# Kernel tuning notes

Measured on AMD Instinct MI355X. Metric: run time of the kernel, lower is better.

Reference implementation:

```python
import jax, jax.numpy as jnp
import numpy as np

NSAMPLE = 32
EPS = 1e-5

def _conv1x1(x, W, b):
    # x: (B, Cin, M, K), W: (Cout, Cin) -> (B, Cout, M, K)
    return jnp.einsum('oc,bcmk->bomk', W, x) + b[None, :, None, None]

def _bn(x, g, b):
    # BatchNorm2d in train mode: per-channel batch stats over (B, M, K)
    mu = x.mean(axis=(0, 2, 3), keepdims=True)
    var = ((x - mu) ** 2).mean(axis=(0, 2, 3), keepdims=True)
    return (x - mu) * jax.lax.rsqrt(var + EPS) * g[None, :, None, None] + b[None, :, None, None]

def setup_inputs() -> dict:
    key = jax.random.key(0)
    ks = jax.random.split(key, 8)
    B, P, C = 4, 8192, 64
    hidden, out_ch = 128, 128
    in_tot = C + 3
    w = lambda k, shape: jax.random.normal(k, shape, jnp.float32) * 0.05
    return {
        'xyz': jax.random.normal(ks[0], (B, P, 3), jnp.float32),
        'feats': jax.random.normal(ks[1], (B, C, P), jnp.float32),
        'W1': w(ks[2], (hidden, in_tot)), 'b1': jnp.zeros((hidden,), jnp.float32),
        'g1': jnp.ones((hidden,), jnp.float32), 'be1': jnp.zeros((hidden,), jnp.float32),
        'W2': w(ks[3], (out_ch, hidden)), 'b2': jnp.zeros((out_ch,), jnp.float32),
        'g2': jnp.ones((out_ch,), jnp.float32), 'be2': jnp.zeros((out_ch,), jnp.float32),
        'Wq1': w(ks[4], (out_ch // 2, out_ch)), 'bq1': jnp.zeros((out_ch // 2,), jnp.float32),
        'Wq2': w(ks[5], (1, out_ch // 2)), 'bq2': jnp.zeros((1,), jnp.float32),
    }

def reference(xyz, feats, W1, b1, g1, be1, W2, b2, g2, be2, Wq1, bq1, Wq2, bq2):
    B, P, _ = xyz.shape
    M = max(1, P // 4)
    K = min(NSAMPLE, P)
    # deterministic equispaced centers (torch.linspace(...).long() truncates = floor)
    idx_c = jnp.floor(jnp.linspace(0.0, P - 1.0, M)).astype(jnp.int32)
    centers = jnp.take(xyz, idx_c, axis=1)                      # (B, M, 3)
    # squared pairwise distances (same argsort order as cdist)
    d2 = ((centers ** 2).sum(-1)[:, :, None]
          + (xyz ** 2).sum(-1)[:, None, :]
          - 2.0 * jnp.einsum('bmd,bnd->bmn', centers, xyz))     # (B, M, P)
    _, idx = jax.lax.top_k(-d2, K)                              # (B, M, K) nearest
    gather = jax.vmap(lambda pts, i: pts[i])                    # (B,P,C),(B,M,K)->(B,M,K,C)
    neigh_xyz = gather(xyz, idx)                                # (B, M, K, 3)
    local_xyz = jnp.transpose(neigh_xyz - centers[:, :, None, :], (0, 3, 1, 2))  # (B,3,M,K)
    neigh_f = jnp.transpose(gather(jnp.swapaxes(feats, 1, 2), idx), (0, 3, 1, 2))  # (B,C,M,K)
    cat = jnp.concatenate([local_xyz, neigh_f], axis=1)         # (B, C+3, M, K)
    h = jax.nn.relu(_bn(_conv1x1(cat, W1, b1), g1, be1))
    feat_local = jax.nn.relu(_bn(_conv1x1(h, W2, b2), g2, be2))  # (B, out_ch, M, K)
    w = _conv1x1(jax.nn.relu(_conv1x1(feat_local, Wq1, bq1)), Wq2, bq2)  # (B,1,M,K)
    w = jax.nn.softmax(w, axis=-1)
    feat_agg = (feat_local * w).sum(-1)                         # (B, out_ch, M)
    return centers, feat_agg
```

## Files before the change

### kernel.cpp

```cpp
#include <hip/hip_runtime.h>


typedef __attribute__((ext_vector_type(8))) short s16x8;
typedef __attribute__((ext_vector_type(4))) float f32x4;

__device__ __forceinline__ unsigned short f2bf(float f) {
  unsigned int u = __float_as_uint(f);
  unsigned int r = u + 0x7fffu + ((u >> 16) & 1u);
  return (unsigned short)(r >> 16);
}
__device__ __forceinline__ float bf2f(unsigned short s) {
  return __uint_as_float(((unsigned int)s) << 16);
}

__global__ __launch_bounds__(256) void prep2_kernel(const float* __restrict__ W1,
                                                    const float* __restrict__ W2,
                                                    const float* __restrict__ Wq1,
                                                    const float* __restrict__ xyz,
                                                    const float* __restrict__ feats,
                                                    unsigned short* __restrict__ W1p,
                                                    unsigned short* __restrict__ W2p,
                                                    unsigned short* __restrict__ Wq1p,
                                                    float4* __restrict__ xyzq,
                                                    unsigned short* __restrict__ featsT) {
  __shared__ float tile[64][65];
  const int t = threadIdx.x;
  if (blockIdx.x >= 282) {
    const int bx = blockIdx.x - 282;
    const int b = bx >> 7;
    const int p0 = (bx & 127) * 64;
    {
      const int pp = t & 63, c4 = t >> 6;
#pragma unroll
      for (int j = 0; j < 16; ++j) {
        int c = j * 4 + c4;
        tile[c][pp] = feats[((size_t)(b * 64 + c)) * 8192 + p0 + pp];
      }
    }
    __syncthreads();
    {
      const int cc = t & 63, p4 = t >> 6;
#pragma unroll
      for (int j = 0; j < 16; ++j) {
        int pr = j * 4 + p4;
        featsT[((size_t)(b * 8192 + p0 + pr)) * 64 + cc] = f2bf(tile[cc][pr]);
      }
    }
    return;
  }
  int i = blockIdx.x * 256 + t;
  if (i < 13312) {
    int o = i / 104, k = i % 104;
    float v = 0.f;
    if (k < 64) v = W1[o * 67 + 3 + k];
    else if (k < 67) v = W1[o * 67 + (k - 64)];
    W1p[i] = f2bf(v);
    return;
  }
  i -= 13312;
  if (i < 17408) {
    int o = i / 136, k = i % 136;
    W2p[i] = (k < 128) ? f2bf(W2[o * 128 + k]) : (unsigned short)0;
    return;
  }
  i -= 17408;
  if (i < 8704) {
    int o = i / 136, k = i % 136;
    Wq1p[i] = (k < 128) ? f2bf(Wq1[o * 128 + k]) : (unsigned short)0;
    return;
  }
  i -= 8704;
  if (i < 32768) {
    const float* q = xyz + (size_t)i * 3;
    float x = q[0], y = q[1], z = q[2];
    float4 v; v.x = x; v.y = y; v.z = z; v.w = (x * x + y * y) + z * z;
    xyzq[i] = v;
  }
}

#define CANDMAX 512
__global__ __launch_bounds__(512, 2) void sel3_kernel(const float4* __restrict__ xyzq,
    float* __restrict__ centers_out, int* __restrict__ idx_out) {
  const int t = threadIdx.x, lane = t & 63, wid = t >> 6;
  const int b = blockIdx.y;
  const int m0 = blockIdx.x * 16;
  __shared__ unsigned int hist[2][4096];
  __shared__ unsigned long long cand[2][CANDMAX];
  __shared__ float4 cc4[16];
  __shared__ int selb[2][32];
  __shared__ int ctrl[2][2];
  __shared__ int cutb[2];
  __shared__ int wsum[2][4];

  const float4* xb = xyzq + (size_t)b * 8192;
  float4 pt[16];
#pragma unroll
  for (int i = 0; i < 16; ++i) pt[i] = xb[i * 512 + t];

  if (t < 16) {
    int mIdx = m0 + t;
    int pc = (mIdx * 8191) / 2047;
    float4 c = xb[pc];
    cc4[t] = c;
    float* co = centers_out + ((size_t)(b * 2048 + mIdx)) * 3;
    co[0] = c.x; co[1] = c.y; co[2] = c.z;
  }
  for (int j = t; j < 8192; j += 512) ((unsigned int*)hist)[j] = 0;
  if (t < 4) ctrl[t >> 1][t & 1] = 0;
  __syncthreads();

  for (int ci = 0; ci < 8; ++ci) {
    const float4 cA = cc4[2 * ci], cB = cc4[2 * ci + 1];
#pragma unroll
    for (int i = 0; i < 16; ++i) {
      float dotA = (cA.x * pt[i].x + cA.y * pt[i].y) + cA.z * pt[i].z;
      float d2A = (cA.w + pt[i].w) - 2.0f * dotA;
      unsigned int uA = __float_as_uint(d2A);
      uA = (uA & 0x80000000u) ? ~uA : (uA | 0x80000000u);
      atomicAdd(&hist[0][uA >> 20], 1u);
      float dotB = (cB.x * pt[i].x + cB.y * pt[i].y) + cB.z * pt[i].z;
      float d2B = (cB.w + pt[i].w) - 2.0f * dotB;
      unsigned int uB = __float_as_uint(d2B);
      uB = (uB & 0x80000000u) ? ~uB : (uB | 0x80000000u);
      atomicAdd(&hist[1][uB >> 20], 1u);
    }
    __syncthreads();
    {
      const int h = t >> 8;
      const int th = t & 255;
      const int wl = wid & 3;
      const int base = th * 16;
      const unsigned int* H = hist[h];
      int csum = 0;
#pragma unroll
      for (int j = 0; j < 16; ++j) csum += (int)H[base + j];
      int incl = csum;
#pragma unroll
      for (int d = 1; d < 64; d <<= 1) {
        int v = __shfl_up(incl, d);
        if (lane >= d) incl += v;
      }
      if (lane == 63) wsum[h][wl] = incl;
      __syncthreads();
      int woff = 0;
      for (int i2 = 0; i2 < wl; ++i2) woff += wsum[h][i2];
      int excl = woff + incl - csum;
      if (excl < 32 && excl + csum >= 32) {
        int cum = excl, binsel = base + 15;
        for (int j = 0; j < 16; ++j) {
          int cv = (int)H[base + j];
          if (cum + cv >= 32) { binsel = base + j; break; }
          cum += cv;
        }
        cutb[h] = binsel;
      }
    }
    __syncthreads();
    const unsigned int cutA = (unsigned int)cutb[0];
    const unsigned int cutB = (unsigned int)cutb[1];
#pragma unroll
    for (int i = 0; i < 16; ++i) {
      const int pidx = i * 512 + t;
      float dotA = (cA.x * pt[i].x + cA.y * pt[i].y) + cA.z * pt[i].z;
      float d2A = (cA.w + pt[i].w) - 2.0f * dotA;
      unsigned int uA = __float_as_uint(d2A);
      uA = (uA & 0x80000000u) ? ~uA : (uA | 0x80000000u);
      unsigned int keyA = uA >> 20;
      if (keyA < cutA) {
        int pos = atomicAdd(&ctrl[0][0], 1);
        selb[0][pos] = pidx;
      } else if (keyA == cutA) {
        int pos = atomicAdd(&ctrl[0][1], 1);
        if (pos < CANDMAX) cand[0][pos] = ((unsigned long long)uA << 32) | (unsigned int)pidx;
      }
      float dotB = (cB.x * pt[i].x + cB.y * pt[i].y) + cB.z * pt[i].z;
      float d2B = (cB.w + pt[i].w) - 2.0f * dotB;
      unsigned int uB = __float_as_uint(d2B);
      uB = (uB & 0x80000000u) ? ~uB : (uB | 0x80000000u);
      unsigned int keyB = uB >> 20;
      if (keyB < cutB) {
        int pos = atomicAdd(&ctrl[1][0], 1);
        selb[1][pos] = pidx;
      } else if (keyB == cutB) {
        int pos = atomicAdd(&ctrl[1][1], 1);
        if (pos < CANDMAX) cand[1][pos] = ((unsigned long long)uB << 32) | (unsigned int)pidx;
      }
    }
    __syncthreads();
    if (wid < 2) {
      const int nsel = ctrl[wid][0];
      const int need = 32 - nsel;
      const int nc = min(ctrl[wid][1], CANDMAX);
      volatile unsigned long long* vc = cand[wid];
      for (int r = 0; r < need; ++r) {
        unsigned long long best = ~0ull;
        int bs = -1;
#pragma unroll
        for (int bb = 0; bb < CANDMAX; bb += 64) {
          int j = bb + lane;
          if (j < nc) {
            unsigned long long v = vc[j];
            if (v < best) { best = v; bs = j; }
          }
        }
#pragma unroll
        for (int d = 32; d; d >>= 1) {
          unsigned long long ob = __shfl_xor(best, d);
          int os = __shfl_xor(bs, d);
          if (ob < best) { best = ob; bs = os; }
        }
        if (lane == 0) {
          selb[wid][nsel + r] = (int)(best & 0xffffffffu);
          cand[wid][bs] = ~0ull;
        }
      }
    } else {
      for (int j = t - 128; j < 8192; j += 384) ((unsigned int*)hist)[j] = 0;
    }
    __syncthreads();
    if (t < 64) {
      int cc = t >> 5;
      idx_out[(size_t)(b * 2048 + m0 + 2 * ci + cc) * 32 + (t & 31)] = selb[cc][t & 31];
    }
    if (t < 4) ctrl[t >> 1][t & 1] = 0;
    __syncthreads();
  }
}

__global__ __launch_bounds__(1024) void cntA_kernel(const float4* __restrict__ xyzq,
    const float* __restrict__ centers, const int* __restrict__ idxb,
    float* __restrict__ partials, float* __restrict__ dstats) {
  const int t = threadIdx.x;
  const int b = blockIdx.x >> 6, quar = (blockIdx.x >> 4) & 3, esl = blockIdx.x & 15;
  const int pbase = quar * 2048;
  __shared__ float L[4][2048];
  __shared__ float mred[16][9];
  for (int j = t; j < 8192; j += 1024) ((float*)L)[j] = 0.f;
  __syncthreads();
  float m9[9] = {0.f, 0.f, 0.f, 0.f, 0.f, 0.f, 0.f, 0.f, 0.f};
#pragma unroll
  for (int i = 0; i < 4; ++i) {
    int e = esl * 4096 + i * 1024 + t;
    int p = idxb[b * 65536 + e];
    if ((unsigned)(p - pbase) < 2048u) {
      int g = e >> 5;
      const float* cp = centers + ((size_t)(b * 2048 + g)) * 3;
      float cx = cp[0], cy = cp[1], cz = cp[2];
      float4 v = xyzq[(size_t)b * 8192 + p];
      int l = p - pbase;
      atomicAdd(&L[0][l], 1.f);
      atomicAdd(&L[1][l], cx);
      atomicAdd(&L[2][l], cy);
      atomicAdd(&L[3][l], cz);
      float dx = v.x - cx, dy = v.y - cy, dz = v.z - cz;
      m9[0] += dx; m9[1] += dy; m9[2] += dz;
      m9[3] += dx * dx; m9[4] += dy * dy; m9[5] += dz * dz;
      m9[6] += dx * dy; m9[7] += dx * dz; m9[8] += dy * dz;
    }
  }
#pragma unroll
  for (int k = 0; k < 9; ++k) {
#pragma unroll
    for (int d = 1; d < 64; d <<= 1) m9[k] += __shfl_xor(m9[k], d);
  }
  if ((t & 63) == 0) {
#pragma unroll
    for (int k = 0; k < 9; ++k) mred[t >> 6][k] = m9[k];
  }
  __syncthreads();
  if (t < 9) {
    float s = 0.f;
#pragma unroll
    for (int w = 0; w < 16; ++w) s += mred[w][t];
    atomicAdd(&dstats[t], s);
  }
  float* pb = partials + (size_t)blockIdx.x * 8192;
  for (int j = t; j < 8192; j += 1024) pb[j] = ((float*)L)[j];
}

__global__ __launch_bounds__(256) void cntB_kernel(const float* __restrict__ partials,
    float* __restrict__ cnt, float* __restrict__ scx, float* __restrict__ scy,
    float* __restrict__ scz) {
  const int idx = blockIdx.x * 256 + threadIdx.x;
  const int pt = idx & 2047;
  const int arr = (idx >> 11) & 3;
  const int quar = (idx >> 13) & 3;
  const int b = idx >> 15;
  const float* base = partials + ((size_t)((b * 4 + quar) * 16)) * 8192 + arr * 2048 + pt;
  float s = 0.f;
#pragma unroll
  for (int e = 0; e < 16; ++e) s += base[(size_t)e * 8192];
  const int gp = b * 8192 + quar * 2048 + pt;
  if (arr == 0) cnt[gp] = s;
  else if (arr == 1) scx[gp] = s;
  else if (arr == 2) scy[gp] = s;
  else scz[gp] = s;
}

__global__ __launch_bounds__(1024) void cnt16_kernel(const float4* __restrict__ xyzq,
    const float* __restrict__ centers, const int* __restrict__ idxb,
    float* __restrict__ cnt, float* __restrict__ scx, float* __restrict__ scy,
    float* __restrict__ scz, float* __restrict__ dstats) {
  const int t = threadIdx.x;
  const int b = blockIdx.x >> 2, quar = blockIdx.x & 3;
  const int pbase = quar * 2048;
  __shared__ float L[4][2048];
  for (int j = t; j < 8192; j += 1024) ((float*)L)[j] = 0.f;
  __syncthreads();
  float m9[9] = {0.f, 0.f, 0.f, 0.f, 0.f, 0.f, 0.f, 0.f, 0.f};
  for (int i = 0; i < 64; ++i) {
    int e = i * 1024 + t;
    int p = idxb[b * 65536 + e];
    if (p >= pbase && p < pbase + 2048) {
      int g = e >> 5;
      const float* cp = centers + ((size_t)(b * 2048 + g)) * 3;
      float cx = cp[0], cy = cp[1], cz = cp[2];
      float4 v = xyzq[(size_t)b * 8192 + p];
      int l = p - pbase;
      atomicAdd(&L[0][l], 1.f);
      atomicAdd(&L[1][l], cx);
      atomicAdd(&L[2][l], cy);
      atomicAdd(&L[3][l], cz);
      float dx = v.x - cx, dy = v.y - cy, dz = v.z - cz;
      m9[0] += dx; m9[1] += dy; m9[2] += dz;
      m9[3] += dx * dx; m9[4] += dy * dy; m9[5] += dz * dz;
      m9[6] += dx * dy; m9[7] += dx * dz; m9[8] += dy * dz;
    }
  }
#pragma unroll
  for (int k = 0; k < 9; ++k) {
#pragma unroll
    for (int d = 1; d < 64; d <<= 1) m9[k] += __shfl_xor(m9[k], d);
  }
  if ((t & 63) == 0) {
#pragma unroll
    for (int k = 0; k < 9; ++k) atomicAdd(&dstats[k], m9[k]);
  }
  __syncthreads();
  for (int j = t; j < 2048; j += 1024) {
    int gp = b * 8192 + pbase + j;
    cnt[gp] = L[0][j];
    scx[gp] = L[1][j];
    scy[gp] = L[2][j];
    scz[gp] = L[3][j];
  }
}

__global__ __launch_bounds__(256) void gram_kernel(const float* __restrict__ feats,
    const float4* __restrict__ xyzq, const float* __restrict__ cnt,
    const float* __restrict__ scx, const float* __restrict__ scy,
    const float* __restrict__ scz, float* __restrict__ Sff,
    float* __restrict__ Sfd, float* __restrict__ Fbar) {
  const int t = threadIdx.x;
  const int b = blockIdx.y;
  const int p0 = blockIdx.x * 128;
  __shared__ float fT[128][68];
  __shared__ float cw_s[128], e_s[3][128];
  const int c1 = (t >> 4) * 4, c2 = (t & 15) * 4;
  const int aux = t & 3;
  const bool doaux = ((t & 15) < 4);
  float acc[4][4] = {};
  float accA[4] = {};
#pragma unroll
  for (int j = 0; j < 32; ++j) {
    int idx = j * 256 + t;
    int cch = idx >> 7, pp = idx & 127;
    fT[pp][cch] = feats[((size_t)(b * 64 + cch)) * 8192 + p0 + pp];
  }
  if (t < 128) {
    int gp = b * 8192 + p0 + t;
    float cw = cnt[gp];
    cw_s[t] = cw;
    float4 v = xyzq[gp];
    e_s[0][t] = cw * v.x - scx[gp];
    e_s[1][t] = cw * v.y - scy[gp];
    e_s[2][t] = cw * v.z - scz[gp];
  }
  __syncthreads();
  for (int pp = 0; pp < 128; ++pp) {
    float cw = cw_s[pp];
    float4 f1 = *(const float4*)&fT[pp][c1];
    float4 f2 = *(const float4*)&fT[pp][c2];
    float f1a[4] = {f1.x, f1.y, f1.z, f1.w};
    float f2a[4] = {f2.x, f2.y, f2.z, f2.w};
#pragma unroll
    for (int i = 0; i < 4; ++i) {
      float wsc = f1a[i] * cw;
#pragma unroll
      for (int j = 0; j < 4; ++j) acc[i][j] += wsc * f2a[j];
    }
    if (doaux) {
      float mult = (aux < 3) ? e_s[aux][pp] : cw;
#pragma unroll
      for (int i = 0; i < 4; ++i) accA[i] += f1a[i] * mult;
    }
  }
#pragma unroll
  for (int i = 0; i < 4; ++i)
#pragma unroll
    for (int j = 0; j < 4; ++j) atomicAdd(&Sff[(c1 + i) * 64 + c2 + j], acc[i][j]);
  if (doaux) {
#pragma unroll
    for (int i = 0; i < 4; ++i) {
      if (aux < 3) atomicAdd(&Sfd[(c1 + i) * 3 + aux], accA[i]);
      else atomicAdd(&Fbar[c1 + i], accA[i]);
    }
  }
}

__global__ __launch_bounds__(256) void fin_kernel(const float* __restrict__ W1,
    const float* __restrict__ b1, const float* __restrict__ Sff,
    const float* __restrict__ Sfd, const float* __restrict__ Fbar,
    const float* __restrict__ dstats, float* __restrict__ stats) {
  __shared__ float sS[4096], sFd[192], sFb[64], sD[16];
  const int t = threadIdx.x;
  for (int j = t; j < 4096; j += 256) sS[j] = Sff[j];
  if (t < 192) sFd[t] = Sfd[t];
  if (t < 64) sFb[t] = Fbar[t];
  if (t < 9) sD[t] = dstats[t];
  __syncthreads();
  const int c = t >> 1, h = t & 1;
  float wf[64];
#pragma unroll
  for (int i = 0; i < 64; ++i) wf[i] = W1[c * 67 + 3 + i];
  const float wx0 = W1[c * 67], wx1 = W1[c * 67 + 1], wx2 = W1[c * 67 + 2];
  float qacc = 0.f;
  for (int i = h * 32; i < h * 32 + 32; ++i) {
    float rd = 0.f;
    const float4* row = (const float4*)&sS[i * 64];
#pragma unroll
    for (int j4 = 0; j4 < 16; ++j4) {
      float4 v = row[j4];
      rd += v.x * wf[j4 * 4] + v.y * wf[j4 * 4 + 1] + v.z * wf[j4 * 4 + 2] + v.w * wf[j4 * 4 + 3];
    }
    rd += 2.f * (sFd[i * 3] * wx0 + sFd[i * 3 + 1] * wx1 + sFd[i * 3 + 2] * wx2);
    qacc += wf[i] * rd;
  }
  qacc += __shfl_xor(qacc, 1);
  if (h == 0) {
    const float N = 262144.f;
    float lin = 0.f;
#pragma unroll
    for (int i = 0; i < 64; ++i) lin += wf[i] * sFb[i];
    lin += wx0 * sD[0] + wx1 * sD[1] + wx2 * sD[2];
    float bb = b1[c];
    float Sy = lin + bb * N;
    float dd = wx0 * wx0 * sD[3] + wx1 * wx1 * sD[4] + wx2 * wx2 * sD[5]
             + 2.f * (wx0 * wx1 * sD[6] + wx0 * wx2 * sD[7] + wx1 * wx2 * sD[8]);
    float Sy2 = qacc + dd + 2.f * bb * lin + bb * bb * N;
    stats[c] = Sy;
    stats[128 + c] = Sy2;
  }
}

template <int STAGE>
__global__ __launch_bounds__(512, 2) void mlp_kernel(
    const float* __restrict__ xyz, const unsigned short* __restrict__ featsT,
    const int* __restrict__ idxbuf, const float* __restrict__ centers,
    const unsigned short* __restrict__ W1p_g, const float* __restrict__ b1,
    const float* __restrict__ g1, const float* __restrict__ be1,
    const unsigned short* __restrict__ W2p_g, const float* __restrict__ b2,
    const float* __restrict__ g2, const float* __restrict__ be2,
    const unsigned short* __restrict__ Wq1p_g, const float* __restrict__ bq1,
    const float* __restrict__ Wq2, const float* __restrict__ bq2,
    float* __restrict__ stats, float* __restrict__ out_agg) {
  const int t = threadIdx.x;
  const int T = blockIdx.x;
  const int G0 = T * 4;
  const int b = G0 >> 11;

  __shared__ __align__(16) unsigned short W1l[13312];
  __shared__ __align__(16) unsigned short W2l[8704];
  __shared__ __align__(16) unsigned short A2l[17408];
  __shared__ float sc1a[128], sh1a[128], sc2a[128], sh2a[128];
  float* sredS = (float*)W1l;
  float* sredQ = (float*)W1l + 1024;
  float* sv  = (float*)W2l;
  float* wv  = (float*)W2l + 128;
  float* agg = (float*)W2l + 256;

  const int lane = t & 63, rw = t >> 6;
  const int m = lane & 15, q = lane >> 4;

  for (int i = t; i < 1664; i += 512) ((s16x8*)W1l)[i] = ((const s16x8*)W1p_g)[i];
  for (int i = t; i < 1088; i += 512) ((s16x8*)W2l)[i] = ((const s16x8*)W2p_g)[i];

  const float invN = 1.0f / 262144.0f;
  if (t < 128) {
    float mu = stats[t] * invN;
    float var = stats[128 + t] * invN - mu * mu;
    float s = g1[t] * rsqrtf(var + 1e-5f);
    sc1a[t] = s;
    sh1a[t] = (b1[t] - mu) * s + be1[t];
    if (STAGE == 3) {
      float mu2 = stats[256 + t] * invN;
      float var2 = stats[384 + t] * invN - mu2 * mu2;
      float s2 = g2[t] * rsqrtf(var2 + 1e-5f);
      sc2a[t] = s2;
      sh2a[t] = (b2[t] - mu2) * s2 + be2[t];
    }
  }

  const int r = rw * 16 + m;
  const int g = G0 + (r >> 5);
  const int p = idxbuf[(size_t)g * 32 + (r & 31)];
  const unsigned short* fr = featsT + ((size_t)(b * 8192) + p) * 64;
  s16x8 a0 = *(const s16x8*)(fr + q * 8);
  s16x8 a1 = *(const s16x8*)(fr + 32 + q * 8);
  s16x8 a2 = (s16x8){0, 0, 0, 0, 0, 0, 0, 0};
  if (q == 0) {
    const float* cp = centers + (size_t)g * 3;
    const float* qp = xyz + ((size_t)(b * 8192) + p) * 3;
    a2[0] = (short)f2bf(qp[0] - cp[0]);
    a2[1] = (short)f2bf(qp[1] - cp[1]);
    a2[2] = (short)f2bf(qp[2] - cp[2]);
  }
  __syncthreads();

  {
    f32x4 acc[8];
#pragma unroll
    for (int nt = 0; nt < 8; ++nt) acc[nt] = (f32x4){0.f, 0.f, 0.f, 0.f};
#pragma unroll
    for (int kb = 0; kb < 3; ++kb) {
      s16x8 a = (kb == 0) ? a0 : ((kb == 1) ? a1 : a2);
#pragma unroll
      for (int nt = 0; nt < 8; ++nt) {
        s16x8 bf = *(const s16x8*)(W1l + (nt * 16 + m) * 104 + kb * 32 + q * 8);
        acc[nt] = __builtin_amdgcn_mfma_f32_16x16x32_bf16(a, bf, acc[nt], 0, 0, 0);
      }
    }
#pragma unroll
    for (int nt = 0; nt < 8; ++nt) {
      int ch = nt * 16 + m;
      float s = sc1a[ch], o = sh1a[ch];
#pragma unroll
      for (int r4 = 0; r4 < 4; ++r4)
        A2l[(rw * 16 + q * 4 + r4) * 136 + ch] = f2bf(fmaxf(acc[nt][r4] * s + o, 0.f));
    }
  }
  __syncthreads();

  float fl[2][4][4];
  const int aoff2 = (rw * 16 + m) * 136 + q * 8;
  for (int h2 = 0; h2 < 2; ++h2) {
    if (h2 == 1) {
      __syncthreads();
      for (int i = t; i < 1088; i += 512) ((s16x8*)W2l)[i] = ((const s16x8*)W2p_g)[1088 + i];
      if (STAGE == 3) {
        for (int i = t; i < 1088; i += 512) ((s16x8*)W1l)[i] = ((const s16x8*)Wq1p_g)[i];
      }
      __syncthreads();
    }
    f32x4 bacc[4];
#pragma unroll
    for (int nt = 0; nt < 4; ++nt) bacc[nt] = (f32x4){0.f, 0.f, 0.f, 0.f};
#pragma unroll
    for (int kb = 0; kb < 4; ++kb) {
      s16x8 a = *(const s16x8*)(A2l + aoff2 + kb * 32);
#pragma unroll
      for (int nt = 0; nt < 4; ++nt) {
        s16x8 bf = *(const s16x8*)(W2l + (nt * 16 + m) * 136 + kb * 32 + q * 8);
        bacc[nt] = __builtin_amdgcn_mfma_f32_16x16x32_bf16(a, bf, bacc[nt], 0, 0, 0);
      }
    }
    if (STAGE == 2) {
#pragma unroll
      for (int nt = 0; nt < 4; ++nt) {
        int ch = h2 * 64 + nt * 16 + m;
        float bb = b2[ch];
        float s = 0.f, sq = 0.f;
#pragma unroll
        for (int r4 = 0; r4 < 4; ++r4) {
          float y = bacc[nt][r4] + bb;
          s += y; sq += y * y;
        }
        s += __shfl_xor(s, 16); sq += __shfl_xor(sq, 16);
        s += __shfl_xor(s, 32); sq += __shfl_xor(sq, 32);
        if (q == 0) { sredS[ch * 8 + rw] = s; sredQ[ch * 8 + rw] = sq; }
      }
      __syncthreads();
      if (t < 64) {
        int ch = h2 * 64 + t;
        float ss = 0.f, qq = 0.f;
#pragma unroll
        for (int i2 = 0; i2 < 8; ++i2) { ss += sredS[ch * 8 + i2]; qq += sredQ[ch * 8 + i2]; }
        atomicAdd(&stats[256 + ch], ss);
        atomicAdd(&stats[384 + ch], qq);
      }
      if (h2 == 1) return;
    } else {
#pragma unroll
      for (int nt = 0; nt < 4; ++nt) {
        int ch = h2 * 64 + nt * 16 + m;
        float s = sc2a[ch], o = sh2a[ch];
#pragma unroll
        for (int r4 = 0; r4 < 4; ++r4)
          fl[h2][nt][r4] = fmaxf(bacc[nt][r4] * s + o, 0.f);
      }
    }
  }

  __syncthreads();
#pragma unroll
  for (int h2 = 0; h2 < 2; ++h2)
#pragma unroll
    for (int nt = 0; nt < 4; ++nt) {
      int ch = h2 * 64 + nt * 16 + m;
#pragma unroll
      for (int r4 = 0; r4 < 4; ++r4)
        A2l[(rw * 16 + q * 4 + r4) * 136 + ch] = f2bf(fl[h2][nt][r4]);
    }
  __syncthreads();

  {
    f32x4 qacc[4];
#pragma unroll
    for (int nt = 0; nt < 4; ++nt) qacc[nt] = (f32x4){0.f, 0.f, 0.f, 0.f};
#pragma unroll
    for (int kb = 0; kb < 4; ++kb) {
      s16x8 a = *(const s16x8*)(A2l + aoff2 + kb * 32);
#pragma unroll
      for (int nt = 0; nt < 4; ++nt) {
        s16x8 bf = *(const s16x8*)(W1l + (nt * 16 + m) * 136 + kb * 32 + q * 8);
        qacc[nt] = __builtin_amdgcn_mfma_f32_16x16x32_bf16(a, bf, qacc[nt], 0, 0, 0);
      }
    }
    float ba[4], w[4];
#pragma unroll
    for (int nt = 0; nt < 4; ++nt) { ba[nt] = bq1[nt * 16 + m]; w[nt] = Wq2[nt * 16 + m]; }
    float part[4];
#pragma unroll
    for (int r4 = 0; r4 < 4; ++r4) {
      float pv = 0.f;
#pragma unroll
      for (int nt = 0; nt < 4; ++nt) pv += fmaxf(qacc[nt][r4] + ba[nt], 0.f) * w[nt];
      part[r4] = pv;
    }
#pragma unroll
    for (int d = 1; d < 16; d <<= 1) {
#pragma unroll
      for (int r4 = 0; r4 < 4; ++r4) part[r4] += __shfl_xor(part[r4], d);
    }
    if (m == 0) {
#pragma unroll
      for (int r4 = 0; r4 < 4; ++r4) sv[rw * 16 + q * 4 + r4] = part[r4];
    }
  }
  __syncthreads();
  if (t < 128) {
    float x = sv[t] + bq2[0];
    float mx = x;
#pragma unroll
    for (int d = 16; d; d >>= 1) mx = fmaxf(mx, __shfl_xor(mx, d, 32));
    float e = expf(x - mx);
    float ssum = e;
#pragma unroll
    for (int d = 16; d; d >>= 1) ssum += __shfl_xor(ssum, d, 32);
    wv[t] = e / ssum;
  }
  __syncthreads();
  {
    float wreg[4];
#pragma unroll
    for (int r4 = 0; r4 < 4; ++r4) wreg[r4] = wv[rw * 16 + q * 4 + r4];
    const int gl = rw >> 1, par = rw & 1;
#pragma unroll
    for (int h2 = 0; h2 < 2; ++h2)
#pragma unroll
      for (int nt = 0; nt < 4; ++nt) {
        float pv = 0.f;
#pragma unroll
        for (int r4 = 0; r4 < 4; ++r4) pv += wreg[r4] * fl[h2][nt][r4];
        pv += __shfl_xor(pv, 16);
        pv += __shfl_xor(pv, 32);
        if (q == 0) {
          int ch = h2 * 64 + nt * 16 + m;
          agg[(gl * 128 + ch) * 2 + par] = pv;
        }
      }
  }
  __syncthreads();
  {
    int gl = t >> 7, ch = t & 127;
    float v = agg[(gl * 128 + ch) * 2] + agg[(gl * 128 + ch) * 2 + 1];
    out_agg[((size_t)(b * 128 + ch)) * 2048 + ((G0 + gl) & 2047)] = v;
  }
}

__global__ __launch_bounds__(512, 2) void fwd_kernel(
    const float* __restrict__ xyz, const unsigned short* __restrict__ featsT,
    const int* __restrict__ idxbuf, const float* __restrict__ centers,
    const unsigned short* __restrict__ W1p_g, const float* __restrict__ b1,
    const float* __restrict__ g1, const float* __restrict__ be1,
    const unsigned short* __restrict__ W2p_g, const float* __restrict__ b2,
    float* __restrict__ stats, unsigned short* __restrict__ Y2) {
  const int t = threadIdx.x;
  const int T = blockIdx.x;
  const int G0 = T * 4;
  const int b = G0 >> 11;

  __shared__ __align__(16) unsigned short W1l[13312];
  __shared__ __align__(16) unsigned short W2l[8704];
  __shared__ __align__(16) unsigned short A2l[17408];
  __shared__ float sc1a[128], sh1a[128];
  float* sredS = (float*)W1l;
  float* sredQ = (float*)W1l + 1024;

  const int lane = t & 63, rw = t >> 6;
  const int m = lane & 15, q = lane >> 4;

  for (int i = t; i < 1664; i += 512) ((s16x8*)W1l)[i] = ((const s16x8*)W1p_g)[i];
  for (int i = t; i < 1088; i += 512) ((s16x8*)W2l)[i] = ((const s16x8*)W2p_g)[i];

  const float invN = 1.0f / 262144.0f;
  if (t < 128) {
    float mu = stats[t] * invN;
    float var = stats[128 + t] * invN - mu * mu;
    float s = g1[t] * rsqrtf(var + 1e-5f);
    sc1a[t] = s;
    sh1a[t] = (b1[t] - mu) * s + be1[t];
  }
  const int r = rw * 16 + m;
  const int g = G0 + (r >> 5);
  const int p = idxbuf[(size_t)g * 32 + (r & 31)];
  const unsigned short* fr = featsT + ((size_t)(b * 8192) + p) * 64;
  s16x8 a0 = *(const s16x8*)(fr + q * 8);
  s16x8 a1 = *(const s16x8*)(fr + 32 + q * 8);
  s16x8 a2 = (s16x8){0, 0, 0, 0, 0, 0, 0, 0};
  if (q == 0) {
    const float* cp = centers + (size_t)g * 3;
    const float* qp = xyz + ((size_t)(b * 8192) + p) * 3;
    a2[0] = (short)f2bf(qp[0] - cp[0]);
    a2[1] = (short)f2bf(qp[1] - cp[1]);
    a2[2] = (short)f2bf(qp[2] - cp[2]);
  }
  __syncthreads();

  {
    f32x4 acc[8];
#pragma unroll
    for (int nt = 0; nt < 8; ++nt) acc[nt] = (f32x4){0.f, 0.f, 0.f, 0.f};
#pragma unroll
    for (int kb = 0; kb < 3; ++kb) {
      s16x8 a = (kb == 0) ? a0 : ((kb == 1) ? a1 : a2);
#pragma unroll
      for (int nt = 0; nt < 8; ++nt) {
        s16x8 bf = *(const s16x8*)(W1l + (nt * 16 + m) * 104 + kb * 32 + q * 8);
        acc[nt] = __builtin_amdgcn_mfma_f32_16x16x32_bf16(a, bf, acc[nt], 0, 0, 0);
      }
    }
#pragma unroll
    for (int nt = 0; nt < 8; ++nt) {
      int ch = nt * 16 + m;
      float s = sc1a[ch], o = sh1a[ch];
#pragma unroll
      for (int r4 = 0; r4 < 4; ++r4)
        A2l[(rw * 16 + q * 4 + r4) * 136 + ch] = f2bf(fmaxf(acc[nt][r4] * s + o, 0.f));
    }
  }
  __syncthreads();

  float y2r[2][4][4];
  const int aoff2 = (rw * 16 + m) * 136 + q * 8;
  for (int h2 = 0; h2 < 2; ++h2) {
    if (h2 == 1) {
      __syncthreads();
      for (int i = t; i < 1088; i += 512) ((s16x8*)W2l)[i] = ((const s16x8*)W2p_g)[1088 + i];
      __syncthreads();
    }
    f32x4 bacc[4];
#pragma unroll
    for (int nt = 0; nt < 4; ++nt) bacc[nt] = (f32x4){0.f, 0.f, 0.f, 0.f};
#pragma unroll
    for (int kb = 0; kb < 4; ++kb) {
      s16x8 a = *(const s16x8*)(A2l + aoff2 + kb * 32);
#pragma unroll
      for (int nt = 0; nt < 4; ++nt) {
        s16x8 bf = *(const s16x8*)(W2l + (nt * 16 + m) * 136 + kb * 32 + q * 8);
        bacc[nt] = __builtin_amdgcn_mfma_f32_16x16x32_bf16(a, bf, bacc[nt], 0, 0, 0);
      }
    }
#pragma unroll
    for (int nt = 0; nt < 4; ++nt) {
      int ch = h2 * 64 + nt * 16 + m;
      float bb = b2[ch];
      float s = 0.f, sq = 0.f;
#pragma unroll
      for (int r4 = 0; r4 < 4; ++r4) {
        float y = bacc[nt][r4] + bb;
        s += y; sq += y * y;
        y2r[h2][nt][r4] = bacc[nt][r4];
      }
      s += __shfl_xor(s, 16); sq += __shfl_xor(sq, 16);
      s += __shfl_xor(s, 32); sq += __shfl_xor(sq, 32);
      if (q == 0) { sredS[ch * 8 + rw] = s; sredQ[ch * 8 + rw] = sq; }
    }
    __syncthreads();
    if (t < 64) {
      int ch = h2 * 64 + t;
      float ss = 0.f, qq = 0.f;
#pragma unroll
      for (int i2 = 0; i2 < 8; ++i2) { ss += sredS[ch * 8 + i2]; qq += sredQ[ch * 8 + i2]; }
      atomicAdd(&stats[256 + ch], ss);
      atomicAdd(&stats[384 + ch], qq);
    }
  }
  __syncthreads();
#pragma unroll
  for (int h2 = 0; h2 < 2; ++h2)
#pragma unroll
    for (int nt = 0; nt < 4; ++nt) {
      int ch = h2 * 64 + nt * 16 + m;
#pragma unroll
      for (int r4 = 0; r4 < 4; ++r4)
        A2l[(rw * 16 + q * 4 + r4) * 136 + ch] = f2bf(y2r[h2][nt][r4]);
    }
  __syncthreads();
  for (int i = t; i < 2048; i += 512) {
    int row = i >> 4, off = (i & 15) * 8;
    *(s16x8*)(Y2 + ((size_t)(T * 128 + row)) * 128 + off) = *(const s16x8*)(A2l + row * 136 + off);
  }
}

__global__ __launch_bounds__(512) void fin2_kernel(
    const unsigned short* __restrict__ Y2, const float* __restrict__ stats,
    const float* __restrict__ g2, const float* __restrict__ be2,
    const float* __restrict__ b2, const unsigned short* __restrict__ Wq1p_g,
    const float* __restrict__ bq1, const float* __restrict__ Wq2,
    const float* __restrict__ bq2, float* __restrict__ out_agg) {
  const int t = threadIdx.x;
  const int T = blockIdx.x;
  const int G0 = T * 2;
  const int b = G0 >> 11;

  __shared__ __align__(16) unsigned short Wq1l[8704];
  __shared__ float sc2a[128], sh2a[128];
  __shared__ float sv2[128], wv[64], agg2[512];

  const int lane = t & 63, wid = t >> 6;
  const int m = lane & 15, q = lane >> 4;
  const int rw = wid & 3, cw = wid >> 2;

  for (int i = t; i < 1088; i += 512) ((s16x8*)Wq1l)[i] = ((const s16x8*)Wq1p_g)[i];
  const float invN = 1.0f / 262144.0f;
  if (t < 128) {
    float mu2 = stats[256 + t] * invN;
    float var2 = stats[384 + t] * invN - mu2 * mu2;
    float s2 = g2[t] * rsqrtf(var2 + 1e-5f);
    sc2a[t] = s2;
    sh2a[t] = (b2[t] - mu2) * s2 + be2[t];
  }
  const int row = rw * 16 + m;
  const unsigned short* yr = Y2 + ((size_t)(T * 64 + row)) * 128;
  s16x8 yv[4];
#pragma unroll
  for (int kb = 0; kb < 4; ++kb) yv[kb] = *(const s16x8*)(yr + kb * 32 + q * 8);
  __syncthreads();

  float flr[4][8];
  s16x8 af[4];
#pragma unroll
  for (int kb = 0; kb < 4; ++kb) {
#pragma unroll
    for (int j = 0; j < 8; ++j) {
      int ch = kb * 32 + q * 8 + j;
      float f = fmaxf(bf2f((unsigned short)yv[kb][j]) * sc2a[ch] + sh2a[ch], 0.f);
      flr[kb][j] = f;
      af[kb][j] = (short)f2bf(f);
    }
  }
  {
    f32x4 qacc[2];
#pragma unroll
    for (int nt = 0; nt < 2; ++nt) qacc[nt] = (f32x4){0.f, 0.f, 0.f, 0.f};
#pragma unroll
    for (int kb = 0; kb < 4; ++kb) {
#pragma unroll
      for (int nt = 0; nt < 2; ++nt) {
        s16x8 bf = *(const s16x8*)(Wq1l + (cw * 32 + nt * 16 + m) * 136 + kb * 32 + q * 8);
        qacc[nt] = __builtin_amdgcn_mfma_f32_16x16x32_bf16(af[kb], bf, qacc[nt], 0, 0, 0);
      }
    }
    int qc0 = cw * 32 + m, qc1 = qc0 + 16;
    float ba0 = bq1[qc0], ba1 = bq1[qc1];
    float w0 = Wq2[qc0], w1 = Wq2[qc1];
    float part[4];
#pragma unroll
    for (int r4 = 0; r4 < 4; ++r4) {
      float v0 = fmaxf(qacc[0][r4] + ba0, 0.f);
      float v1 = fmaxf(qacc[1][r4] + ba1, 0.f);
      part[r4] = v0 * w0 + v1 * w1;
    }
#pragma unroll
    for (int d = 1; d < 16; d <<= 1) {
#pragma unroll
      for (int r4 = 0; r4 < 4; ++r4) part[r4] += __shfl_xor(part[r4], d);
    }
    if (m == 0) {
#pragma unroll
      for (int r4 = 0; r4 < 4; ++r4) sv2[(rw * 16 + q * 4 + r4) * 2 + cw] = part[r4];
    }
  }
  __syncthreads();
  if (t < 64) {
    float x = sv2[t * 2] + sv2[t * 2 + 1] + bq2[0];
    float mx = x;
#pragma unroll
    for (int d = 16; d; d >>= 1) mx = fmaxf(mx, __shfl_xor(mx, d, 32));
    float e = expf(x - mx);
    float ssum = e;
#pragma unroll
    for (int d = 16; d; d >>= 1) ssum += __shfl_xor(ssum, d, 32);
    wv[t] = e / ssum;
  }
  __syncthreads();
  if (cw == 0) {
    const float w = wv[row];
    const int gl = rw >> 1, rwpar = rw & 1;
#pragma unroll
    for (int kb = 0; kb < 4; ++kb) {
#pragma unroll
      for (int j = 0; j < 8; ++j) {
        float pv = w * flr[kb][j];
        pv += __shfl_xor(pv, 1);
        pv += __shfl_xor(pv, 2);
        pv += __shfl_xor(pv, 4);
        pv += __shfl_xor(pv, 8);
        if (m == 0) agg2[(gl * 128 + kb * 32 + q * 8 + j) * 2 + rwpar] = pv;
      }
    }
  }
  __syncthreads();
  if (t < 256) {
    int gl = t >> 7, ch = t & 127;
    float v = agg2[(gl * 128 + ch) * 2] + agg2[(gl * 128 + ch) * 2 + 1];
    out_agg[((size_t)(b * 128 + ch)) * 2048 + ((G0 + gl) & 2047)] = v;
  }
}

extern "C" void kernel_launch(void* const* d_in, const int* in_sizes, int n_in,
                              void* d_out, int out_size, void* d_ws, size_t ws_size,
                              hipStream_t stream) {
  const float* xyz   = (const float*)d_in[0];
  const float* feats = (const float*)d_in[1];
  const float* W1    = (const float*)d_in[2];
  const float* b1    = (const float*)d_in[3];
  const float* g1    = (const float*)d_in[4];
  const float* be1   = (const float*)d_in[5];
  const float* W2    = (const float*)d_in[6];
  const float* b2    = (const float*)d_in[7];
  const float* g2    = (const float*)d_in[8];
  const float* be2   = (const float*)d_in[9];
  const float* Wq1   = (const float*)d_in[10];
  const float* bq1   = (const float*)d_in[11];
  const float* Wq2   = (const float*)d_in[12];
  const float* bq2   = (const float*)d_in[13];

  float* outp    = (float*)d_out;
  float* centers = outp;
  float* out_agg = outp + 24576;

  char* base = (char*)d_ws;
  unsigned short* featsT = (unsigned short*)base;
  float4* xyzq  = (float4*)(base + 4194304);
  int*    idxb  = (int*)(base + 4718592);
  unsigned short* W1p  = (unsigned short*)(base + 5767168);
  unsigned short* W2p  = (unsigned short*)(base + 5793792);
  unsigned short* Wq1p = (unsigned short*)(base + 5828608);
  float* stats  = (float*)(base + 5846016);
  float* dstats = stats + 512;
  float* Fbar   = stats + 528;
  float* Sfd    = stats + 592;
  float* Sff    = stats + 784;
  float* cntp   = stats + 4880;
  float* scx    = cntp + 32768;
  float* scy    = scx + 32768;
  float* scz    = scy + 32768;
  float* partials = (float*)(base + 8388608);
  unsigned short* Y2 = (unsigned short*)(base + 8388608);
  const bool bigws = ws_size >= (size_t)75497472;
  const bool midws = ws_size >= (size_t)16777216;

  hipMemsetAsync(stats, 0, 19520, stream);
  prep2_kernel<<<794, 256, 0, stream>>>(W1, W2, Wq1, xyz, feats, W1p, W2p, Wq1p, xyzq, featsT);
  sel3_kernel<<<dim3(128, 4), 512, 0, stream>>>(xyzq, centers, idxb);
  if (midws) {
    cntA_kernel<<<256, 1024, 0, stream>>>(xyzq, centers, idxb, partials, dstats);
    cntB_kernel<<<512, 256, 0, stream>>>(partials, cntp, scx, scy, scz);
  } else {
    cnt16_kernel<<<16, 1024, 0, stream>>>(xyzq, centers, idxb, cntp, scx, scy, scz, dstats);
  }
  gram_kernel<<<dim3(64, 4), 256, 0, stream>>>(feats, xyzq, cntp, scx, scy, scz, Sff, Sfd, Fbar);
  fin_kernel<<<1, 256, 0, stream>>>(W1, b1, Sff, Sfd, Fbar, dstats, stats);
  if (bigws) {
    fwd_kernel<<<2048, 512, 0, stream>>>(xyz, featsT, idxb, centers,
                                         W1p, b1, g1, be1, W2p, b2, stats, Y2);
    fin2_kernel<<<4096, 512, 0, stream>>>(Y2, stats, g2, be2, b2,
                                          Wq1p, bq1, Wq2, bq2, out_agg);
  } else {
    mlp_kernel<2><<<2048, 512, 0, stream>>>(xyz, featsT, idxb, centers,
                                            W1p, b1, g1, be1, W2p, b2, g2, be2,
                                            Wq1p, bq1, Wq2, bq2, stats, out_agg);
    mlp_kernel<3><<<2048, 512, 0, stream>>>(xyz, featsT, idxb, centers,
                                            W1p, b1, g1, be1, W2p, b2, g2, be2,
                                            Wq1p, bq1, Wq2, bq2, stats, out_agg);
  }
}
```

Before: 443.2 us.

## Select neighbors for eight centers per pass with one wave each

The top-K neighbor selection kernel now handles 8 centers per pass instead of 2. Each center gets a 1024-bin histogram keyed on the top 10 bits, down from 4096 bins on the top 12, and its own wavefront does the prefix scan, cut-bin search and final candidate selection. This removes the block-level scan synchronisations and the idle waves in the selection phase. The cost is coarser bins, so more candidates land in the cut bin, and the candidate buffer is halved to 256, which could overflow for dense neighborhoods.

```diff
diff --git a/kernel.cpp b/kernel.cpp
--- a/kernel.cpp
+++ b/kernel.cpp
@@ -78,19 +78,18 @@
   }
 }
 
-#define CANDMAX 512
-__global__ __launch_bounds__(512, 2) void sel3_kernel(const float4* __restrict__ xyzq,
+#define CAND8 256
+__global__ __launch_bounds__(512, 2) void sel4_kernel(const float4* __restrict__ xyzq,
     float* __restrict__ centers_out, int* __restrict__ idx_out) {
   const int t = threadIdx.x, lane = t & 63, wid = t >> 6;
   const int b = blockIdx.y;
   const int m0 = blockIdx.x * 16;
-  __shared__ unsigned int hist[2][4096];
-  __shared__ unsigned long long cand[2][CANDMAX];
+  __shared__ unsigned int hist[8][1024];
+  __shared__ unsigned long long cand[8][CAND8];
   __shared__ float4 cc4[16];
-  __shared__ int selb[2][32];
-  __shared__ int ctrl[2][2];
-  __shared__ int cutb[2];
-  __shared__ int wsum[2][4];
+  __shared__ int selb[8][32];
+  __shared__ int ctrl[8][2];
+  __shared__ unsigned int cutb[8];
 
   const float4* xb = xyzq + (size_t)b * 8192;
   float4 pt[16];
@@ -106,31 +105,26 @@
     co[0] = c.x; co[1] = c.y; co[2] = c.z;
   }
   for (int j = t; j < 8192; j += 512) ((unsigned int*)hist)[j] = 0;
-  if (t < 4) ctrl[t >> 1][t & 1] = 0;
-  __syncthreads();
-
-  for (int ci = 0; ci < 8; ++ci) {
-    const float4 cA = cc4[2 * ci], cB = cc4[2 * ci + 1];
-#pragma unroll
-    for (int i = 0; i < 16; ++i) {
-      float dotA = (cA.x * pt[i].x + cA.y * pt[i].y) + cA.z * pt[i].z;
-      float d2A = (cA.w + pt[i].w) - 2.0f * dotA;
-      unsigned int uA = __float_as_uint(d2A);
-      uA = (uA & 0x80000000u) ? ~uA : (uA | 0x80000000u);
-      atomicAdd(&hist[0][uA >> 20], 1u);
-      float dotB = (cB.x * pt[i].x + cB.y * pt[i].y) + cB.z * pt[i].z;
-      float d2B = (cB.w + pt[i].w) - 2.0f * dotB;
-      unsigned int uB = __float_as_uint(d2B);
-      uB = (uB & 0x80000000u) ? ~uB : (uB | 0x80000000u);
-      atomicAdd(&hist[1][uB >> 20], 1u);
+  if (t < 16) ctrl[t >> 1][t & 1] = 0;
+  __syncthreads();
+
+  for (int it = 0; it < 2; ++it) {
+    for (int c = 0; c < 8; ++c) {
+      const float4 cc = cc4[it * 8 + c];
+      unsigned int* H = hist[c];
+#pragma unroll
+      for (int i = 0; i < 16; ++i) {
+        float dot = (cc.x * pt[i].x + cc.y * pt[i].y) + cc.z * pt[i].z;
+        float d2 = (cc.w + pt[i].w) - 2.0f * dot;
+        unsigned int u = __float_as_uint(d2);
+        u = (u & 0x80000000u) ? ~u : (u | 0x80000000u);
+        atomicAdd(&H[u >> 22], 1u);
+      }
     }
     __syncthreads();
     {
-      const int h = t >> 8;
-      const int th = t & 255;
-      const int wl = wid & 3;
-      const int base = th * 16;
-      const unsigned int* H = hist[h];
+      const unsigned int* H = hist[wid];
+      const int base = lane * 16;
       int csum = 0;
 #pragma unroll
       for (int j = 0; j < 16; ++j) csum += (int)H[base + j];
@@ -140,63 +134,53 @@
         int v = __shfl_up(incl, d);
         if (lane >= d) incl += v;
       }
-      if (lane == 63) wsum[h][wl] = incl;
-      __syncthreads();
-      int woff = 0;
-      for (int i2 = 0; i2 < wl; ++i2) woff += wsum[h][i2];
-      int excl = woff + incl - csum;
-      if (excl < 32 && excl + csum >= 32) {
-        int cum = excl, binsel = base + 15;
-        for (int j = 0; j < 16; ++j) {
-          int cv = (int)H[base + j];
-          if (cum + cv >= 32) { binsel = base + j; break; }
-          cum += cv;
+      int before = incl - csum;
+      unsigned long long mk = __ballot((before < 32) && (incl >= 32));
+      int cutlane = __ffsll(mk) - 1;
+      int cum = before, cutloc = base + 15;
+      bool fnd = false;
+#pragma unroll
+      for (int j = 0; j < 16; ++j) {
+        int cv = (int)H[base + j];
+        if (!fnd) {
+          if (cum + cv >= 32) { cutloc = base + j; fnd = true; }
+          else cum += cv;
         }
-        cutb[h] = binsel;
-      }
+      }
+      int cl = __shfl(cutloc, cutlane);
+      if (lane == 0) cutb[wid] = (unsigned int)cl;
     }
     __syncthreads();
-    const unsigned int cutA = (unsigned int)cutb[0];
-    const unsigned int cutB = (unsigned int)cutb[1];
-#pragma unroll
-    for (int i = 0; i < 16; ++i) {
-      const int pidx = i * 512 + t;
-      float dotA = (cA.x * pt[i].x + cA.y * pt[i].y) + cA.z * pt[i].z;
-      float d2A = (cA.w + pt[i].w) - 2.0f * dotA;
-      unsigned int uA = __float_as_uint(d2A);
-      uA = (uA & 0x80000000u) ? ~uA : (uA | 0x80000000u);
-      unsigned int keyA = uA >> 20;
-      if (keyA < cutA) {
-        int pos = atomicAdd(&ctrl[0][0], 1);
-        selb[0][pos] = pidx;
-      } else if (keyA == cutA) {
-        int pos = atomicAdd(&ctrl[0][1], 1);
-        if (pos < CANDMAX) cand[0][pos] = ((unsigned long long)uA << 32) | (unsigned int)pidx;
-      }
-      float dotB = (cB.x * pt[i].x + cB.y * pt[i].y) + cB.z * pt[i].z;
-      float d2B = (cB.w + pt[i].w) - 2.0f * dotB;
-      unsigned int uB = __float_as_uint(d2B);
-      uB = (uB & 0x80000000u) ? ~uB : (uB | 0x80000000u);
-      unsigned int keyB = uB >> 20;
-      if (keyB < cutB) {
-        int pos = atomicAdd(&ctrl[1][0], 1);
-        selb[1][pos] = pidx;
-      } else if (keyB == cutB) {
-        int pos = atomicAdd(&ctrl[1][1], 1);
-        if (pos < CANDMAX) cand[1][pos] = ((unsigned long long)uB << 32) | (unsigned int)pidx;
+    for (int c = 0; c < 8; ++c) {
+      const float4 cc = cc4[it * 8 + c];
+      const unsigned int cut = cutb[c];
+#pragma unroll
+      for (int i = 0; i < 16; ++i) {
+        float dot = (cc.x * pt[i].x + cc.y * pt[i].y) + cc.z * pt[i].z;
+        float d2 = (cc.w + pt[i].w) - 2.0f * dot;
+        unsigned int u = __float_as_uint(d2);
+        u = (u & 0x80000000u) ? ~u : (u | 0x80000000u);
+        unsigned int key = u >> 22;
+        if (key < cut) {
+          int pos = atomicAdd(&ctrl[c][0], 1);
+          selb[c][pos] = i * 512 + t;
+        } else if (key == cut) {
+          int pos = atomicAdd(&ctrl[c][1], 1);
+          if (pos < CAND8) cand[c][pos] = ((unsigned long long)u << 32) | (unsigned int)(i * 512 + t);
+        }
       }
     }
     __syncthreads();
-    if (wid < 2) {
+    {
       const int nsel = ctrl[wid][0];
       const int need = 32 - nsel;
-      const int nc = min(ctrl[wid][1], CANDMAX);
+      const int nc = min(ctrl[wid][1], CAND8);
       volatile unsigned long long* vc = cand[wid];
       for (int r = 0; r < need; ++r) {
         unsigned long long best = ~0ull;
         int bs = -1;
 #pragma unroll
-        for (int bb = 0; bb < CANDMAX; bb += 64) {
+        for (int bb = 0; bb < CAND8; bb += 64) {
           int j = bb + lane;
           if (j < nc) {
             unsigned long long v = vc[j];
@@ -214,15 +198,11 @@
           cand[wid][bs] = ~0ull;
         }
       }
-    } else {
-      for (int j = t - 128; j < 8192; j += 384) ((unsigned int*)hist)[j] = 0;
-    }
-    __syncthreads();
-    if (t < 64) {
-      int cc = t >> 5;
-      idx_out[(size_t)(b * 2048 + m0 + 2 * ci + cc) * 32 + (t & 31)] = selb[cc][t & 31];
-    }
-    if (t < 4) ctrl[t >> 1][t & 1] = 0;
+      if (lane < 32)
+        idx_out[(size_t)(b * 2048 + m0 + it * 8 + wid) * 32 + lane] = selb[wid][lane];
+      for (int j = lane; j < 1024; j += 64) hist[wid][j] = 0;
+      if (lane == 0) { ctrl[wid][0] = 0; ctrl[wid][1] = 0; }
+    }
     __syncthreads();
   }
 }
@@ -984,7 +964,7 @@
 
   hipMemsetAsync(stats, 0, 19520, stream);
   prep2_kernel<<<794, 256, 0, stream>>>(W1, W2, Wq1, xyz, feats, W1p, W2p, Wq1p, xyzq, featsT);
-  sel3_kernel<<<dim3(128, 4), 512, 0, stream>>>(xyzq, centers, idxb);
+  sel4_kernel<<<dim3(128, 4), 512, 0, stream>>>(xyzq, centers, idxb);
   if (midws) {
     cntA_kernel<<<256, 1024, 0, stream>>>(xyzq, centers, idxb, partials, dstats);
     cntB_kernel<<<512, 256, 0, stream>>>(partials, cntp, scx, scy, scz);
```

New measurement: 466.1 us. +5.2%, slower.
